# Kernel tuning notes

Measured on AMD Instinct MI355X. Metric: run time of the kernel, lower is better.

Reference implementation:

```python
import jax, jax.numpy as jnp
import numpy as np

D = 1024
H = 16
HD = D // H
EPS = 1e-5

def gelu_tanh(x):
    c = jnp.sqrt(jnp.asarray(2.0 / jnp.pi, x.dtype))
    return 0.5 * x * (1.0 + jnp.tanh(c * (x + 0.044715 * x ** 3)))

def layernorm(x, scale, shift):
    mean = x.mean(axis=-1, keepdims=True)
    var = x.var(axis=-1, keepdims=True)  # biased, matches unbiased=False
    return scale * (x - mean) / jnp.sqrt(var + EPS) + shift

def setup_inputs() -> dict:
    key = jax.random.key(0)
    ks = jax.random.split(key, 12)
    s = 0.02
    return {
        "x": jax.random.normal(ks[0], (2, 2048, D), jnp.float32),
        "Wq": jax.random.normal(ks[1], (D, D), jnp.float32) * s,
        "Wk": jax.random.normal(ks[2], (D, D), jnp.float32) * s,
        "Wv": jax.random.normal(ks[3], (D, D), jnp.float32) * s,
        "Wo": jax.random.normal(ks[4], (D, D), jnp.float32) * s,
        "bo": jnp.zeros((D,), jnp.float32),
        "W1": jax.random.normal(ks[5], (D, 4 * D), jnp.float32) * s,
        "b1": jnp.zeros((4 * D,), jnp.float32),
        "W2": jax.random.normal(ks[6], (4 * D, D), jnp.float32) * s,
        "b2": jnp.zeros((D,), jnp.float32),
        "g1": jnp.ones((D,), jnp.float32),
        "s1": jnp.zeros((D,), jnp.float32),
        "g2": jnp.ones((D,), jnp.float32),
        "s2": jnp.zeros((D,), jnp.float32),
    }

def reference(x, Wq, Wk, Wv, Wo, bo, W1, b1, W2, b2, g1, s1, g2, s2):
    B, S, _ = x.shape
    # --- attention sublayer (pre-LN) ---
    shortcut = x
    h = layernorm(x, g1, s1)
    q = (h @ Wq).reshape(B, S, H, HD).transpose(0, 2, 1, 3)  # bhsd
    k = (h @ Wk).reshape(B, S, H, HD).transpose(0, 2, 1, 3)
    v = (h @ Wv).reshape(B, S, H, HD).transpose(0, 2, 1, 3)
    scores = jnp.einsum('bhqd,bhkd->bhqk', q, k)
    causal = jnp.tril(jnp.ones((S, S), bool))
    scores = jnp.where(causal, scores, -jnp.inf)
    attn = jax.nn.softmax(scores / np.sqrt(HD), axis=-1)
    ctx = jnp.einsum('bhqk,bhkd->bhqd', attn, v)
    ctx = ctx.transpose(0, 2, 1, 3).reshape(B, S, D)
    x = ctx @ Wo + bo + shortcut
    # --- FFN sublayer (pre-LN) ---
    shortcut = x
    h = layernorm(x, g2, s2)
    h = gelu_tanh(h @ W1 + b1) @ W2 + b2
    return h + shortcut
```

## Files before the change

### kernel.cpp

```cpp
#include <hip/hip_runtime.h>
#include <hip/hip_bf16.h>
#include <math.h>

typedef __bf16 bf16;
typedef __bf16 bf16x4 __attribute__((ext_vector_type(4)));
typedef __bf16 bf16x8 __attribute__((ext_vector_type(8)));
typedef float f32x4 __attribute__((ext_vector_type(4)));

#define DEV static __device__ __forceinline__

constexpr int Dm = 1024;
constexpr int Sq = 2048;
constexpr int Mrows = 4096;
constexpr size_t AE = (size_t)Mrows * Dm;

DEV void gload_lds16(const void* g, void* l) {
  __builtin_amdgcn_global_load_lds((const __attribute__((address_space(1))) unsigned int*)g,
                                   (__attribute__((address_space(3))) unsigned int*)l,
                                   16, 0, 0);
}

DEV float gelu_f(float u) {
  const float c = 0.7978845608028654f;
  float t = c * (u + 0.044715f * u * u * u);
  return u / (1.0f + __expf(-2.0f * t));
}

__global__ void transpose_split_kernel(const float* __restrict__ W,
                                       bf16* __restrict__ Thi,
                                       int K, int N) {
  __shared__ float tile[64][65];
  const int t = threadIdx.x;
  const int nt = blockIdx.x * 64, kt = blockIdx.y * 64;
  #pragma unroll
  for (int i = 0; i < 16; ++i) {
    int id = i * 256 + t;
    int r = id >> 6, c = id & 63;
    tile[r][c] = W[(size_t)(kt + r) * N + nt + c];
  }
  __syncthreads();
  #pragma unroll
  for (int i = 0; i < 16; ++i) {
    int id = i * 256 + t;
    int n = id >> 6, k = id & 63;
    Thi[(size_t)(nt + n) * K + kt + k] = (bf16)tile[k][n];
  }
}

__global__ void ln_kernel(const float* __restrict__ x,
                          const float* __restrict__ gamma, const float* __restrict__ beta,
                          bf16* __restrict__ ohi) {
  const int row = blockIdx.x, t = threadIdx.x;
  const float4 v = ((const float4*)(x + (size_t)row * Dm))[t];
  float s = v.x + v.y + v.z + v.w;
  float sq = v.x * v.x + v.y * v.y + v.z * v.z + v.w * v.w;
  #pragma unroll
  for (int off = 1; off < 64; off <<= 1) {
    s += __shfl_xor(s, off);
    sq += __shfl_xor(sq, off);
  }
  __shared__ float red[8];
  const int wave = t >> 6, lane = t & 63;
  if (lane == 0) { red[wave] = s; red[4 + wave] = sq; }
  __syncthreads();
  s = red[0] + red[1] + red[2] + red[3];
  sq = red[4] + red[5] + red[6] + red[7];
  const float mean = s * (1.0f / 1024.0f);
  const float var = sq * (1.0f / 1024.0f) - mean * mean;
  const float inv = 1.0f / sqrtf(var + 1e-5f);
  const float4 g4 = ((const float4*)gamma)[t];
  const float4 b4 = ((const float4*)beta)[t];
  bf16x4 hv;
  hv[0] = (bf16)((v.x - mean) * inv * g4.x + b4.x);
  hv[1] = (bf16)((v.y - mean) * inv * g4.y + b4.y);
  hv[2] = (bf16)((v.z - mean) * inv * g4.z + b4.z);
  hv[3] = (bf16)((v.w - mean) * inv * g4.w + b4.w);
  ((bf16x4*)(ohi + (size_t)row * Dm))[t] = hv;
}

template<int EP>
__global__ __launch_bounds__(256, 6) void gemm_kernel(
    const bf16* __restrict__ Ahi,
    const bf16* __restrict__ Bthi,
    int K, int N,
    bf16* __restrict__ Ohi,
    float* __restrict__ Of,
    const float* __restrict__ bias, const float* __restrict__ resid) {
  const int t = threadIdx.x, wave = t >> 6, lane = t & 63;
  const int wr = wave >> 1, wc = wave & 1;
  const int l15 = lane & 15, l4 = lane >> 4;
  const int nwg = gridDim.x * gridDim.y;
  const int p0 = blockIdx.y * gridDim.x + blockIdx.x;
  const int swz = (p0 & 7) * (nwg >> 3) + (p0 >> 3);
  const int row0 = (swz / gridDim.x) * 64, col0 = (swz % gridDim.x) * 128;

  __shared__ __align__(16) bf16 sAh[64 * 64];
  __shared__ __align__(16) bf16 sBh[128 * 64];

  f32x4 acc[2][4];
  #pragma unroll
  for (int m = 0; m < 2; ++m)
    #pragma unroll
    for (int n = 0; n < 4; ++n)
      acc[m][n] = (f32x4){0.f, 0.f, 0.f, 0.f};

  for (int kt = 0; kt < K; kt += 64) {
    #pragma unroll
    for (int p = 0; p < 2; ++p) {
      int id = p * 256 + t;
      int r = id >> 3, c = id & 7;
      int cs = (c ^ (r & 7)) << 3;
      gload_lds16(Ahi + (size_t)(row0 + r) * K + kt + cs,
                  (char*)sAh + (p * 256 + wave * 64) * 16);
    }
    #pragma unroll
    for (int p = 0; p < 4; ++p) {
      int id = p * 256 + t;
      int r = id >> 3, c = id & 7;
      int cs = (c ^ (r & 7)) << 3;
      gload_lds16(Bthi + (size_t)(col0 + r) * K + kt + cs,
                  (char*)sBh + (p * 256 + wave * 64) * 16);
    }
    __syncthreads();

    bf16x8 afh[2][2], bfh[4][2];
    #pragma unroll
    for (int m = 0; m < 2; ++m)
      #pragma unroll
      for (int ks = 0; ks < 2; ++ks) {
        int r = wr * 32 + m * 16 + l15;
        int ch = ((ks * 4 + l4) ^ (r & 7)) << 3;
        afh[m][ks] = *(const bf16x8*)&sAh[r * 64 + ch];
      }
    #pragma unroll
    for (int n = 0; n < 4; ++n)
      #pragma unroll
      for (int ks = 0; ks < 2; ++ks) {
        int r = wc * 64 + n * 16 + l15;
        int ch = ((ks * 4 + l4) ^ (r & 7)) << 3;
        bfh[n][ks] = *(const bf16x8*)&sBh[r * 64 + ch];
      }
    #pragma unroll
    for (int ks = 0; ks < 2; ++ks)
      #pragma unroll
      for (int m = 0; m < 2; ++m)
        #pragma unroll
        for (int n = 0; n < 4; ++n)
          acc[m][n] = __builtin_amdgcn_mfma_f32_16x16x32_bf16(afh[m][ks], bfh[n][ks], acc[m][n], 0, 0, 0);
    __syncthreads();
  }

  #pragma unroll
  for (int m = 0; m < 2; ++m)
    #pragma unroll
    for (int n = 0; n < 4; ++n)
      #pragma unroll
      for (int rr = 0; rr < 4; ++rr) {
        int row = row0 + wr * 32 + m * 16 + l4 * 4 + rr;
        int col = col0 + wc * 64 + n * 16 + l15;
        float v = acc[m][n][rr];
        if constexpr (EP == 0) {
          int which = col >> 10;
          int c = col & 1023;
          if (which == 0) {
            float q = v * 0.18033688011111793f;
            bf16 hi = (bf16)q;
            size_t ad = (size_t)row * Dm + c;
            Ohi[ad] = hi; Ohi[AE + ad] = (bf16)(q - (float)hi);
          } else if (which == 1) {
            size_t ad = (size_t)row * Dm + c;
            Ohi[2 * AE + ad] = (bf16)v;
          } else {
            size_t ad = ((size_t)(row >> 11) * Dm + c) * Sq + (row & (Sq - 1));
            Ohi[4 * AE + ad] = (bf16)v;
          }
        } else if constexpr (EP == 1) {
          size_t ad = (size_t)row * N + col;
          Of[ad] = v + bias[col] + resid[ad];
        } else {
          size_t ad = (size_t)row * N + col;
          Ohi[ad] = (bf16)gelu_f(v + bias[col]);
        }
      }
}

__global__ __launch_bounds__(256, 4) void attn_kernel(
    const bf16* __restrict__ qhi, const bf16* __restrict__ qlo,
    const bf16* __restrict__ khi, const bf16* __restrict__ vthi,
    bf16* __restrict__ chi) {
  const int t = threadIdx.x, wave = t >> 6, lane = t & 63;
  const int l15 = lane & 15, l4 = lane >> 4;
  const int i = blockIdx.x;
  const int xcd = i & 7, j = i >> 3;
  const int hl = j & 3, qidx = j >> 2;
  int qt;
  if (qidx < 8)       qt = 31 - qidx;
  else if (qidx < 16) qt = qidx - 8;
  else if (qidx < 24) qt = 39 - qidx;
  else                qt = qidx - 16;
  const int bh = xcd * 4 + hl;
  const int b = bh >> 4, h = bh & 15;
  const int qb = qt * 64;
  const int q0 = qb + wave * 16;

  __shared__ __align__(16) bf16 sK[2][4096], sV[2][4096], sP[4096];

  bf16x8 qfh[2], qfl[2];
  #pragma unroll
  for (int ks = 0; ks < 2; ++ks) {
    size_t ad = (size_t)(b * Sq + q0 + l15) * Dm + h * 64 + ks * 32 + l4 * 8;
    qfh[ks] = *(const bf16x8*)&qhi[ad];
    qfl[ks] = *(const bf16x8*)&qlo[ad];
  }

  f32x4 cacc[4];
  float mrun[4], lrun[4];
  #pragma unroll
  for (int nd = 0; nd < 4; ++nd) cacc[nd] = (f32x4){0.f, 0.f, 0.f, 0.f};
  #pragma unroll
  for (int rr = 0; rr < 4; ++rr) { mrun[rr] = -3e38f; lrun[rr] = 0.f; }

  auto STAGE = [&](int bb, int kb) {
    #pragma unroll
    for (int p = 0; p < 2; ++p) {
      int id = p * 256 + t;
      int r = id >> 3, c = id & 7;
      int cc = (c ^ (r & 7)) << 3;
      size_t ka = (size_t)(b * Sq + kb + r) * Dm + h * 64 + cc;
      size_t va = (size_t)(b * Dm + h * 64 + r) * Sq + kb + cc;
      gload_lds16(&khi[ka], (char*)&sK[bb][0] + (p * 256 + wave * 64) * 16);
      gload_lds16(&vthi[va], (char*)&sV[bb][0] + (p * 256 + wave * 64) * 16);
    }
  };

  STAGE(0, 0);
  __syncthreads();
  int cur = 0;

  for (int kb = 0; kb <= qb; kb += 64) {
    if (kb + 64 <= qb) STAGE(cur ^ 1, kb + 64);

    f32x4 sacc[4];
    #pragma unroll
    for (int nk = 0; nk < 4; ++nk) sacc[nk] = (f32x4){0.f, 0.f, 0.f, 0.f};
    {
      bf16x8 kf[4][2];
      #pragma unroll
      for (int nk = 0; nk < 4; ++nk)
        #pragma unroll
        for (int ks = 0; ks < 2; ++ks) {
          int r = nk * 16 + l15;
          int ch = ((ks * 4 + l4) ^ (r & 7)) << 3;
          kf[nk][ks] = *(const bf16x8*)&sK[cur][r * 64 + ch];
        }
      #pragma unroll
      for (int ks = 0; ks < 2; ++ks)
        #pragma unroll
        for (int nk = 0; nk < 4; ++nk)
          sacc[nk] = __builtin_amdgcn_mfma_f32_16x16x32_bf16(qfh[ks], kf[nk][ks], sacc[nk], 0, 0, 0);
      #pragma unroll
      for (int ks = 0; ks < 2; ++ks)
        #pragma unroll
        for (int nk = 0; nk < 4; ++nk)
          sacc[nk] = __builtin_amdgcn_mfma_f32_16x16x32_bf16(qfl[ks], kf[nk][ks], sacc[nk], 0, 0, 0);
    }

    const bool diag = (kb == qb);
    #pragma unroll
    for (int rr = 0; rr < 4; ++rr) {
      float mx = -3e38f;
      #pragma unroll
      for (int nk = 0; nk < 4; ++nk) {
        float tv = sacc[nk][rr];
        if (diag && (nk * 16 + l15 > wave * 16 + l4 * 4 + rr)) tv = -3e38f;
        sacc[nk][rr] = tv;
        mx = fmaxf(mx, tv);
      }
      mx = fmaxf(mx, __shfl_xor(mx, 1));
      mx = fmaxf(mx, __shfl_xor(mx, 2));
      mx = fmaxf(mx, __shfl_xor(mx, 4));
      mx = fmaxf(mx, __shfl_xor(mx, 8));
      float mold = mrun[rr];
      if (mx > mold + 8.0f) {
        float corr = exp2f(mold - mx);
        lrun[rr] *= corr;
        #pragma unroll
        for (int nd = 0; nd < 4; ++nd) cacc[nd][rr] *= corr;
        mrun[rr] = mx;
        mold = mx;
      }
      float rs = 0.f;
      #pragma unroll
      for (int nk = 0; nk < 4; ++nk) {
        float p = exp2f(sacc[nk][rr] - mold);
        sacc[nk][rr] = p;
        rs += p;
      }
      rs += __shfl_xor(rs, 1);
      rs += __shfl_xor(rs, 2);
      rs += __shfl_xor(rs, 4);
      rs += __shfl_xor(rs, 8);
      lrun[rr] += rs;
    }

    #pragma unroll
    for (int nk = 0; nk < 4; ++nk)
      #pragma unroll
      for (int rr = 0; rr < 4; ++rr) {
        int row = wave * 16 + l4 * 4 + rr;
        int col = nk * 16 + l15;
        int ad = row * 64 + (((col >> 3) ^ (row & 7)) << 3) + (col & 7);
        sP[ad] = (bf16)sacc[nk][rr];
      }

    {
      bf16x8 pf[2];
      #pragma unroll
      for (int ks = 0; ks < 2; ++ks) {
        int r = wave * 16 + l15;
        int ch = ((ks * 4 + l4) ^ (r & 7)) << 3;
        pf[ks] = *(const bf16x8*)&sP[r * 64 + ch];
      }
      bf16x8 vf[2][4];
      #pragma unroll
      for (int ks = 0; ks < 2; ++ks)
        #pragma unroll
        for (int nd = 0; nd < 4; ++nd) {
          int r = nd * 16 + l15;
          int ch = ((ks * 4 + l4) ^ (r & 7)) << 3;
          vf[ks][nd] = *(const bf16x8*)&sV[cur][r * 64 + ch];
        }
      #pragma unroll
      for (int ks = 0; ks < 2; ++ks)
        #pragma unroll
        for (int nd = 0; nd < 4; ++nd)
          cacc[nd] = __builtin_amdgcn_mfma_f32_16x16x32_bf16(pf[ks], vf[ks][nd], cacc[nd], 0, 0, 0);
    }
    __syncthreads();
    cur ^= 1;
  }

  #pragma unroll
  for (int rr = 0; rr < 4; ++rr) {
    float rcp = 1.0f / lrun[rr];
    int qr = q0 + l4 * 4 + rr;
    #pragma unroll
    for (int nd = 0; nd < 4; ++nd) {
      float ov = cacc[nd][rr] * rcp;
      size_t ad = (size_t)(b * Sq + qr) * Dm + h * 64 + nd * 16 + l15;
      chi[ad] = (bf16)ov;
    }
  }
}

extern "C" void kernel_launch(void* const* d_in, const int* in_sizes, int n_in,
                              void* d_out, int out_size, void* d_ws, size_t ws_size,
                              hipStream_t stream) {
  const float* x  = (const float*)d_in[0];
  const float* Wq = (const float*)d_in[1];
  const float* Wk = (const float*)d_in[2];
  const float* Wv = (const float*)d_in[3];
  const float* Wo = (const float*)d_in[4];
  const float* bo = (const float*)d_in[5];
  const float* W1 = (const float*)d_in[6];
  const float* b1 = (const float*)d_in[7];
  const float* W2 = (const float*)d_in[8];
  const float* b2 = (const float*)d_in[9];
  const float* g1 = (const float*)d_in[10];
  const float* s1 = (const float*)d_in[11];
  const float* g2 = (const float*)d_in[12];
  const float* s2 = (const float*)d_in[13];
  float* out = (float*)d_out;

  if (ws_size < 150994944ULL) return;

  char* ws = (char*)d_ws;
  bf16* wqkvT_hi = (bf16*)(ws + 0);
  bf16* woT_hi   = (bf16*)(ws + 12582912);
  bf16* w1T_hi   = (bf16*)(ws + 16777216);
  bf16* w2T_hi   = (bf16*)(ws + 33554432);
  char* rA = ws + 50331648;
  bf16* h_hi  = (bf16*)(rA + 0);
  bf16* q_hi  = (bf16*)(rA + 16777216);
  bf16* q_lo  = (bf16*)(rA + 25165824);
  bf16* k_hi  = (bf16*)(rA + 33554432);
  bf16* vT_hi = (bf16*)(rA + 50331648);
  bf16* a1_hi = (bf16*)(rA + 0);
  char* rB = ws + 117440512;
  bf16* ctx_hi = (bf16*)(rB + 0);
  bf16* h2_hi  = (bf16*)(rB + 0);
  float* x1 = (float*)(ws + 134217728);

  transpose_split_kernel<<<dim3(16, 16), 256, 0, stream>>>(Wq, wqkvT_hi, 1024, 1024);
  transpose_split_kernel<<<dim3(16, 16), 256, 0, stream>>>(Wk, wqkvT_hi + 1024 * 1024, 1024, 1024);
  transpose_split_kernel<<<dim3(16, 16), 256, 0, stream>>>(Wv, wqkvT_hi + 2048 * 1024, 1024, 1024);
  transpose_split_kernel<<<dim3(16, 16), 256, 0, stream>>>(Wo, woT_hi, 1024, 1024);
  transpose_split_kernel<<<dim3(64, 16), 256, 0, stream>>>(W1, w1T_hi, 1024, 4096);
  transpose_split_kernel<<<dim3(16, 64), 256, 0, stream>>>(W2, w2T_hi, 4096, 1024);

  ln_kernel<<<4096, 256, 0, stream>>>(x, g1, s1, h_hi);

  gemm_kernel<0><<<dim3(24, 64), 256, 0, stream>>>(h_hi, wqkvT_hi,
                                                   1024, 3072, q_hi, nullptr, nullptr, nullptr);
  attn_kernel<<<dim3(1024), 256, 0, stream>>>(q_hi, q_lo, k_hi, vT_hi, ctx_hi);

  gemm_kernel<1><<<dim3(8, 64), 256, 0, stream>>>(ctx_hi, woT_hi,
                                                  1024, 1024, nullptr, x1, bo, x);
  ln_kernel<<<4096, 256, 0, stream>>>(x1, g2, s2, h2_hi);

  gemm_kernel<2><<<dim3(32, 64), 256, 0, stream>>>(h2_hi, w1T_hi,
                                                   1024, 4096, a1_hi, nullptr, b1, nullptr);
  gemm_kernel<1><<<dim3(8, 64), 256, 0, stream>>>(a1_hi, w2T_hi,
                                                  4096, 1024, nullptr, out, b2, x1);
}
```

Baseline: 408.4 us.

## Single-buffer attention LDS, raise occupancy, add MFMA priority, merge QKVO transposes

```diff
diff --git a/kernel.cpp b/kernel.cpp
--- a/kernel.cpp
+++ b/kernel.cpp
@@ -24,6 +24,30 @@
   const float c = 0.7978845608028654f;
   float t = c * (u + 0.044715f * u * u * u);
   return u / (1.0f + __expf(-2.0f * t));
+}
+
+__global__ void transpose_qkvo_kernel(const float* __restrict__ Wq, const float* __restrict__ Wk,
+                                      const float* __restrict__ Wv, const float* __restrict__ Wo,
+                                      bf16* __restrict__ Tqkv, bf16* __restrict__ To) {
+  const int z = blockIdx.z;
+  const float* W = (z == 0) ? Wq : (z == 1) ? Wk : (z == 2) ? Wv : Wo;
+  bf16* T = (z < 3) ? (Tqkv + (size_t)z * 1024 * 1024) : To;
+  __shared__ float tile[64][65];
+  const int t = threadIdx.x;
+  const int nt = blockIdx.x * 64, kt = blockIdx.y * 64;
+  #pragma unroll
+  for (int i = 0; i < 16; ++i) {
+    int id = i * 256 + t;
+    int r = id >> 6, c = id & 63;
+    tile[r][c] = W[(size_t)(kt + r) * 1024 + nt + c];
+  }
+  __syncthreads();
+  #pragma unroll
+  for (int i = 0; i < 16; ++i) {
+    int id = i * 256 + t;
+    int n = id >> 6, k = id & 63;
+    T[(size_t)(nt + n) * 1024 + kt + k] = (bf16)tile[k][n];
+  }
 }
 
 __global__ void transpose_split_kernel(const float* __restrict__ W,
@@ -184,7 +208,7 @@
       }
 }
 
-__global__ __launch_bounds__(256, 4) void attn_kernel(
+__global__ __launch_bounds__(256, 6) void attn_kernel(
     const bf16* __restrict__ qhi, const bf16* __restrict__ qlo,
     const bf16* __restrict__ khi, const bf16* __restrict__ vthi,
     bf16* __restrict__ chi) {
@@ -193,17 +217,13 @@
   const int i = blockIdx.x;
   const int xcd = i & 7, j = i >> 3;
   const int hl = j & 3, qidx = j >> 2;
-  int qt;
-  if (qidx < 8)       qt = 31 - qidx;
-  else if (qidx < 16) qt = qidx - 8;
-  else if (qidx < 24) qt = 39 - qidx;
-  else                qt = qidx - 16;
+  const int qt = 31 - qidx;
   const int bh = xcd * 4 + hl;
   const int b = bh >> 4, h = bh & 15;
   const int qb = qt * 64;
   const int q0 = qb + wave * 16;
 
-  __shared__ __align__(16) bf16 sK[2][4096], sV[2][4096], sP[4096];
+  __shared__ __align__(16) bf16 sK[4096], sV[4096], sP[4096];
 
   bf16x8 qfh[2], qfl[2];
   #pragma unroll
@@ -220,7 +240,7 @@
   #pragma unroll
   for (int rr = 0; rr < 4; ++rr) { mrun[rr] = -3e38f; lrun[rr] = 0.f; }
 
-  auto STAGE = [&](int bb, int kb) {
+  for (int kb = 0; kb <= qb; kb += 64) {
     #pragma unroll
     for (int p = 0; p < 2; ++p) {
       int id = p * 256 + t;
@@ -228,17 +248,10 @@
       int cc = (c ^ (r & 7)) << 3;
       size_t ka = (size_t)(b * Sq + kb + r) * Dm + h * 64 + cc;
       size_t va = (size_t)(b * Dm + h * 64 + r) * Sq + kb + cc;
-      gload_lds16(&khi[ka], (char*)&sK[bb][0] + (p * 256 + wave * 64) * 16);
-      gload_lds16(&vthi[va], (char*)&sV[bb][0] + (p * 256 + wave * 64) * 16);
-    }
-  };
-
-  STAGE(0, 0);
-  __syncthreads();
-  int cur = 0;
-
-  for (int kb = 0; kb <= qb; kb += 64) {
-    if (kb + 64 <= qb) STAGE(cur ^ 1, kb + 64);
+      gload_lds16(&khi[ka], (char*)sK + (p * 256 + wave * 64) * 16);
+      gload_lds16(&vthi[va], (char*)sV + (p * 256 + wave * 64) * 16);
+    }
+    __syncthreads();
 
     f32x4 sacc[4];
     #pragma unroll
@@ -251,8 +264,9 @@
         for (int ks = 0; ks < 2; ++ks) {
           int r = nk * 16 + l15;
           int ch = ((ks * 4 + l4) ^ (r & 7)) << 3;
-          kf[nk][ks] = *(const bf16x8*)&sK[cur][r * 64 + ch];
+          kf[nk][ks] = *(const bf16x8*)&sK[r * 64 + ch];
         }
+      __builtin_amdgcn_s_setprio(1);
       #pragma unroll
       for (int ks = 0; ks < 2; ++ks)
         #pragma unroll
@@ -263,6 +277,7 @@
         #pragma unroll
         for (int nk = 0; nk < 4; ++nk)
           sacc[nk] = __builtin_amdgcn_mfma_f32_16x16x32_bf16(qfl[ks], kf[nk][ks], sacc[nk], 0, 0, 0);
+      __builtin_amdgcn_s_setprio(0);
     }
 
     const bool diag = (kb == qb);
@@ -328,16 +343,17 @@
         for (int nd = 0; nd < 4; ++nd) {
           int r = nd * 16 + l15;
           int ch = ((ks * 4 + l4) ^ (r & 7)) << 3;
-          vf[ks][nd] = *(const bf16x8*)&sV[cur][r * 64 + ch];
+          vf[ks][nd] = *(const bf16x8*)&sV[r * 64 + ch];
         }
+      __builtin_amdgcn_s_setprio(1);
       #pragma unroll
       for (int ks = 0; ks < 2; ++ks)
         #pragma unroll
         for (int nd = 0; nd < 4; ++nd)
           cacc[nd] = __builtin_amdgcn_mfma_f32_16x16x32_bf16(pf[ks], vf[ks][nd], cacc[nd], 0, 0, 0);
+      __builtin_amdgcn_s_setprio(0);
     }
     __syncthreads();
-    cur ^= 1;
   }
 
   #pragma unroll
@@ -391,10 +407,7 @@
   bf16* h2_hi  = (bf16*)(rB + 0);
   float* x1 = (float*)(ws + 134217728);
 
-  transpose_split_kernel<<<dim3(16, 16), 256, 0, stream>>>(Wq, wqkvT_hi, 1024, 1024);
-  transpose_split_kernel<<<dim3(16, 16), 256, 0, stream>>>(Wk, wqkvT_hi + 1024 * 1024, 1024, 1024);
-  transpose_split_kernel<<<dim3(16, 16), 256, 0, stream>>>(Wv, wqkvT_hi + 2048 * 1024, 1024, 1024);
-  transpose_split_kernel<<<dim3(16, 16), 256, 0, stream>>>(Wo, woT_hi, 1024, 1024);
+  transpose_qkvo_kernel<<<dim3(16, 16, 4), 256, 0, stream>>>(Wq, Wk, Wv, Wo, wqkvT_hi, woT_hi);
   transpose_split_kernel<<<dim3(64, 16), 256, 0, stream>>>(W1, w1T_hi, 1024, 4096);
   transpose_split_kernel<<<dim3(16, 64), 256, 0, stream>>>(W2, w2T_hi, 4096, 1024);
 
```

Result: slower. 549.8 us (+34.6%).
